# Kernel tuning notes

Measured on AMD Instinct MI355X. Metric: run time of the kernel, lower is better.

## Reference

```python
import jax, jax.numpy as jnp
import numpy as np

N, T, NC, D = 256, 20, 1, 32
NF, Q, VSTEPS, HDYN = 16, 32, 10, 256
HDIM = NF * 64           # n_filt * 4**3
DT = 0.1
BETA = 1.0
LOG2PI = float(np.log(2.0 * np.pi))


def conv2d(x, w, b):
    # k=4, s=2, p=1 : halves spatial dims. x: [B,Cin,H,W], w: [Cout,Cin,4,4]
    y = jax.lax.conv_general_dilated(x, w, (2, 2), [(1, 1), (1, 1)],
                                     dimension_numbers=('NCHW', 'OIHW', 'NCHW'))
    return y + b[None, :, None, None]


def deconv2d(x, w, b):
    # stride-2 transposed conv, doubles spatial dims. w: [Cout,Cin,4,4]
    y = jax.lax.conv_transpose(x, w, (2, 2), 'SAME',
                               dimension_numbers=('NCHW', 'OIHW', 'NCHW'))
    return y + b[None, :, None, None]


def encode(x, C1, c1, C2, c2, C3, c3, Wm, bm, Wl, bl):
    h = jax.nn.relu(conv2d(x, C1, c1))
    h = jax.nn.relu(conv2d(h, C2, c2))
    h = jax.nn.relu(conv2d(h, C3, c3))   # [B, 4*NF, 4, 4]
    h = h.reshape(h.shape[0], -1)        # [B, HDIM]
    return h @ Wm + bm, h @ Wl + bl


def setup_inputs() -> dict:
    key = jax.random.key(0)
    ks = jax.random.split(key, 40)
    r = lambda i, shape, s=0.05: s * jax.random.normal(ks[i], shape, jnp.float32)
    inp = {
        'X': jax.random.uniform(ks[0], (N, T, NC, D, D), jnp.float32),
        'eps_s0': jax.random.normal(ks[1], (N, Q), jnp.float32),
        'eps_v0': jax.random.normal(ks[2], (N, Q), jnp.float32),
        # enc_s (input = 1 frame)
        'Cs1': r(3, (NF, NC, 4, 4)), 'cs1': jnp.zeros((NF,)),
        'Cs2': r(4, (2 * NF, NF, 4, 4)), 'cs2': jnp.zeros((2 * NF,)),
        'Cs3': r(5, (4 * NF, 2 * NF, 4, 4)), 'cs3': jnp.zeros((4 * NF,)),
        'Wsm': r(6, (HDIM, Q)), 'bsm': jnp.zeros((Q,)),
        'Wsl': r(7, (HDIM, Q), 0.01), 'bsl': -1.0 * jnp.ones((Q,)),
        # enc_v (input = v_steps frames stacked as channels)
        'Cv1': r(8, (NF, VSTEPS * NC, 4, 4)), 'cv1': jnp.zeros((NF,)),
        'Cv2': r(9, (2 * NF, NF, 4, 4)), 'cv2': jnp.zeros((2 * NF,)),
        'Cv3': r(10, (4 * NF, 2 * NF, 4, 4)), 'cv3': jnp.zeros((4 * NF,)),
        'Wvm': r(11, (HDIM, Q)), 'bvm': jnp.zeros((Q,)),
        'Wvl': r(12, (HDIM, Q), 0.01), 'bvl': -1.0 * jnp.ones((Q,)),
        # dynamics f : R^{2q} -> R^q (tanh MLP)
        'W1': r(13, (2 * Q, HDYN), 0.1), 'b1': jnp.zeros((HDYN,)),
        'W2': r(14, (HDYN, Q), 0.1), 'b2': jnp.zeros((Q,)),
        # fc3 + decoder
        'Wf': r(15, (Q, HDIM)), 'bf': jnp.zeros((HDIM,)),
        'D1': r(16, (2 * NF, 4 * NF, 4, 4)), 'd1': jnp.zeros((2 * NF,)),
        'D2': r(17, (NF, 2 * NF, 4, 4)), 'd2': jnp.zeros((NF,)),
        'D3': r(18, (NC, NF, 4, 4)), 'd3': jnp.zeros((NC,)),
        'Ndata': 10000,
    }
    return inp


def reference(X, eps_s0, eps_v0,
              Cs1, cs1, Cs2, cs2, Cs3, cs3, Wsm, bsm, Wsl, bsl,
              Cv1, cv1, Cv2, cv2, Cv3, cv3, Wvm, bvm, Wvl, bvl,
              W1, b1, W2, b2, Wf, bf, D1, d1, D2, d2, D3, d3, Ndata):
    Nb, Tt = X.shape[0], X.shape[1]
    # ---- encode z0 = [v0, s0]
    s0_mu, s0_lv = encode(X[:, 0], Cs1, cs1, Cs2, cs2, Cs3, cs3, Wsm, bsm, Wsl, bsl)
    xv = X[:, :VSTEPS].reshape(Nb, VSTEPS * NC, D, D)
    v0_mu, v0_lv = encode(xv, Cv1, cv1, Cv2, cv2, Cv3, cv3, Wvm, bvm, Wvl, bvl)
    s0 = s0_mu + eps_s0 * jnp.exp(s0_lv)
    v0 = v0_mu + eps_v0 * jnp.exp(v0_lv)
    # standard-normal density of the base noise (q dims each)
    logp0 = (-0.5 * jnp.sum(eps_s0 ** 2, -1) - 0.5 * Q * LOG2PI) + \
            (-0.5 * jnp.sum(eps_v0 ** 2, -1) - 0.5 * Q * LOG2PI)
    z0 = jnp.concatenate([v0, s0], axis=1)               # [N,2q]
    qz0_m = jnp.concatenate([v0_mu, s0_mu], axis=1)
    qz0_logv = jnp.concatenate([v0_lv, s0_lv], axis=1)

    # ---- augmented ODE rhs: dz = [f(z), v], dlogp = -tr(df/dv)
    # exact trace for the tanh MLP: J = W2^T diag(1-h^2) W1^T, so
    # tr_{i<q} J = (1-h^2) @ c with c_k = sum_{i<q} W1[i,k] * W2[k,i]
    c = jnp.sum(W1[:Q] * W2.T, axis=0)                   # [HDYN]

    def rhs(vs):
        h = jnp.tanh(vs @ W1 + b1)                       # [N,HDYN]
        dv = h @ W2 + b2                                 # [N,q]
        dvs = jnp.concatenate([dv, vs[:, :Q]], axis=1)   # [N,2q]
        tr = (1.0 - h * h) @ c                           # [N]
        return dvs, -tr

    def rk4_step(carry, _):
        z, lp = carry
        k1z, k1l = rhs(z)
        k2z, k2l = rhs(z + 0.5 * DT * k1z)
        k3z, k3l = rhs(z + 0.5 * DT * k2z)
        k4z, k4l = rhs(z + DT * k3z)
        z2 = z + (DT / 6.0) * (k1z + 2 * k2z + 2 * k3z + k4z)
        lp2 = lp + (DT / 6.0) * (k1l + 2 * k2l + 2 * k3l + k4l)
        return (z2, lp2), (z2, lp2)

    (_, _), (zs, lps) = jax.lax.scan(rk4_step, (z0, logp0), None, length=Tt - 1)
    zt = jnp.concatenate([z0[None], zs], axis=0)         # [T,N,2q]
    logp = jnp.concatenate([logp0[None], lps], axis=0)   # [T,N]
    ztL = jnp.transpose(zt, (1, 0, 2))[None]             # [1,N,T,2q] (L=1)
    logpL = logp.T[None]                                 # [1,N,T]

    # ---- decode positions s_t
    s = ztL[..., Q:].reshape(-1, Q) @ Wf + bf            # [N*T, HDIM]
    h = s.reshape(-1, 4 * NF, 4, 4)
    h = jax.nn.relu(deconv2d(h, D1, d1))                 # [N*T,2NF,8,8]
    h = jax.nn.relu(deconv2d(h, D2, d2))                 # [N*T,NF,16,16]
    Xrec = jax.nn.sigmoid(deconv2d(h, D3, d3))           # [N*T,NC,32,32]
    Xrec = Xrec.reshape(1, Nb, Tt, NC, D, D)

    # ---- ELBO
    log_pzt = -0.5 * jnp.sum(ztL ** 2, -1) - Q * LOG2PI  # N(0,I) over 2q dims
    kl_z = (logpL - log_pzt).sum(2).mean(0)              # [N]
    lhood_L = jnp.log(0.001 + Xrec) * X[None] + jnp.log(1.001 - Xrec) * (1.0 - X[None])
    lhood = lhood_L.sum((2, 3, 4, 5)).mean(0)            # [N]
    kl_w = 0.5 * (jnp.sum(W1 ** 2) + jnp.sum(W2 ** 2))
    Nd = jnp.float32(Ndata)
    lh = Nd * lhood.mean()
    klz = Nd * kl_z.mean()
    elbo = lh - klz - BETA * kl_w
    return Xrec, qz0_m, qz0_logv, ztL, elbo, lh, klz, BETA * kl_w


if __name__ == '__main__':
    outs = reference(**setup_inputs())
    print(outs[0].shape, float(outs[4]))
```

## Files before the change

### kernel.cpp

```cpp
#include <hip/hip_runtime.h>
#include <math.h>

#define N_S 256
#define T_S 20
#define D_S 32
#define NF_S 16
#define Q_S 32
#define HDYN_S 256
#define HDIM_S 1024
#define VSTEPS_S 10
#define DT_S 0.1f
#define LOG2PI_F 1.8378770664093453f

#define OUT_XREC 0
#define OUT_QM   5242880
#define OUT_QLV  5259264
#define OUT_ZT   5275648
#define OUT_SCAL 5603328

#define WS_A1    0
#define WS_A3    0
#define WS_WT1   0
#define WS_WT2   32768
#define WS_WT3   40960
#define WS_A2    1048576
#define WS_S0MU  1572864
#define WS_S0LV  1581056
#define WS_V0MU  1589248
#define WS_V0LV  1597440
#define WS_LOGP  1605632
#define WS_LHOOD 1610752
#define WS_KLZ   1611008
#define WS_KLW   1611264
#define WS_TC    1611520
#define TC_S1 (WS_TC + 0)
#define TC_V1 (WS_TC + 256)
#define TC_S2 (WS_TC + 2816)
#define TC_V2 (WS_TC + 11008)
#define TC_S3 (WS_TC + 19200)
#define TC_V3 (WS_TC + 51968)

__device__ inline void enc_tr(const float* __restrict__ src, float* __restrict__ dst,
                              int e, int CI, int CO) {
    int co = e % CO; int r = e / CO; int tap = r & 15; int ci = r >> 4;
    dst[e] = src[(co * CI + ci) * 16 + tap];
}
__device__ inline void dec_tr(const float* __restrict__ src, float* __restrict__ dst,
                              int e, int CI, int CO) {
    int co = e % CO; int r = e / CO; int ci = r % CI; int tap = r / CI;
    dst[e] = src[(co * CI + ci) * 16 + tap];
}

__global__ __launch_bounds__(256) void prep_enc(
    const float* __restrict__ Cs1, const float* __restrict__ Cv1,
    const float* __restrict__ Cs2, const float* __restrict__ Cv2,
    const float* __restrict__ Cs3, const float* __restrict__ Cv3,
    float* __restrict__ ws)
{
    int idx = blockIdx.x * 256 + threadIdx.x;
    if (blockIdx.x == 0) ws[WS_LHOOD + threadIdx.x] = 0.f;
    if (idx < 256)        enc_tr(Cs1, ws + TC_S1, idx,          1, 16);
    else if (idx < 2816)  enc_tr(Cv1, ws + TC_V1, idx - 256,   10, 16);
    else if (idx < 11008) enc_tr(Cs2, ws + TC_S2, idx - 2816,  16, 32);
    else if (idx < 19200) enc_tr(Cv2, ws + TC_V2, idx - 11008, 16, 32);
    else if (idx < 51968) enc_tr(Cs3, ws + TC_S3, idx - 19200, 32, 64);
    else if (idx < 84736) enc_tr(Cv3, ws + TC_V3, idx - 51968, 32, 64);
}

template<int CIN>
__global__ __launch_bounds__(256) void conv1_lds(
    const float* __restrict__ x, const float* __restrict__ wt,
    const float* __restrict__ bias, float* __restrict__ out)
{
    __shared__ float xin[CIN * 630];
    __shared__ float wl[CIN * 256];
    __shared__ float bl[16];
    int b = blockIdx.x, yh = blockIdx.y, t = threadIdx.x;
    for (int e = t; e < CIN * 576; e += 256) {
        int ci = e / 576;
        int r = (e >> 5) - ci * 18;
        int cx = e & 31;
        int gy = yh * 16 - 1 + r;
        float v = (gy >= 0 && gy < 32) ? x[(size_t)b * 20480 + ci * 1024 + gy * 32 + cx] : 0.f;
        xin[ci * 630 + r * 35 + cx + 1] = v;
    }
    for (int e = t; e < CIN * 18; e += 256) {
        int ci = e / 18, r = e - ci * 18;
        xin[ci * 630 + r * 35 + 0] = 0.f;
        xin[ci * 630 + r * 35 + 33] = 0.f;
    }
    for (int e = t; e < CIN * 256; e += 256) wl[e] = wt[e];
    if (t < 16) bl[t] = bias[t];
    __syncthreads();

    int ocq = t >> 7, p = t & 127;
    int oyl = p >> 4, ox = p & 15;
    float acc[8];
    #pragma unroll
    for (int j = 0; j < 8; j++) acc[j] = bl[ocq * 8 + j];
    for (int ci = 0; ci < CIN; ci++) {
        const float* xc = xin + ci * 630;
        const float* wc = wl + ci * 256 + ocq * 8;
        #pragma unroll
        for (int ky = 0; ky < 4; ky++) {
            const float* xr = xc + (2 * oyl + ky) * 35;
            #pragma unroll
            for (int kx = 0; kx < 4; kx++) {
                float v = xr[2 * ox + kx];
                const float4* w4 = (const float4*)(wc + (ky * 4 + kx) * 16);
                float4 wa = w4[0], wb = w4[1];
                acc[0] = fmaf(v, wa.x, acc[0]);
                acc[1] = fmaf(v, wa.y, acc[1]);
                acc[2] = fmaf(v, wa.z, acc[2]);
                acc[3] = fmaf(v, wa.w, acc[3]);
                acc[4] = fmaf(v, wb.x, acc[4]);
                acc[5] = fmaf(v, wb.y, acc[5]);
                acc[6] = fmaf(v, wb.z, acc[6]);
                acc[7] = fmaf(v, wb.w, acc[7]);
            }
        }
    }
    int oy = yh * 8 + oyl;
    size_t ob = (size_t)b * 4096 + (size_t)(ocq * 8) * 256 + oy * 16 + ox;
    #pragma unroll
    for (int j = 0; j < 8; j++) out[ob + (size_t)j * 256] = fmaxf(acc[j], 0.f);
}

__global__ __launch_bounds__(256) void conv2_lds(
    const float* __restrict__ a1, const float* __restrict__ wt,
    const float* __restrict__ bias, float* __restrict__ out)
{
    __shared__ float xin[16 * 272];
    __shared__ float wl[4096];
    __shared__ float bl[16];
    int b = blockIdx.x, h = blockIdx.y, t = threadIdx.x;
    for (int e = t; e < 4096; e += 256) {
        int ci = e >> 8, r = e & 255, iy = r >> 4, ix = r & 15;
        xin[ci * 272 + iy * 17 + ix] = a1[(size_t)b * 4096 + e];
    }
    for (int e = t; e < 4096; e += 256) {
        int ci = e >> 8, r = e & 255, tap = r >> 4, oc = r & 15;
        wl[e] = wt[ci * 512 + tap * 32 + h * 16 + oc];
    }
    if (t < 16) bl[t] = bias[h * 16 + t];
    __syncthreads();

    int ocq = t >> 6, p = t & 63;
    int pa = p >> 3, pb = p & 7;
    float acc[4];
    #pragma unroll
    for (int j = 0; j < 4; j++) acc[j] = bl[ocq * 4 + j];
    for (int ci = 0; ci < 16; ci++) {
        const float* xc = xin + ci * 272;
        const float* wc = wl + ci * 256 + ocq * 4;
        #pragma unroll
        for (int ky = 0; ky < 4; ky++) {
            int iy = 2 * pa - 1 + ky;
            if ((unsigned)iy >= 16u) continue;
            const float* xr = xc + iy * 17;
            #pragma unroll
            for (int kx = 0; kx < 4; kx++) {
                int ix = 2 * pb - 1 + kx;
                if ((unsigned)ix >= 16u) continue;
                float v = xr[ix];
                float4 wv = *(const float4*)(wc + (ky * 4 + kx) * 16);
                acc[0] = fmaf(v, wv.x, acc[0]);
                acc[1] = fmaf(v, wv.y, acc[1]);
                acc[2] = fmaf(v, wv.z, acc[2]);
                acc[3] = fmaf(v, wv.w, acc[3]);
            }
        }
    }
    size_t ob = (size_t)b * 2048 + (size_t)(h * 16 + ocq * 4) * 64 + pa * 8 + pb;
    #pragma unroll
    for (int j = 0; j < 4; j++) out[ob + (size_t)j * 64] = fmaxf(acc[j], 0.f);
}

__global__ __launch_bounds__(256) void conv3_lds(
    const float* __restrict__ a2, const float* __restrict__ wt,
    const float* __restrict__ bias, float* __restrict__ out)
{
    __shared__ float xin[32 * 72];
    __shared__ float wl[16384];
    __shared__ float bl[32];
    int b = blockIdx.x, h = blockIdx.y, t = threadIdx.x;
    for (int e = t; e < 2048; e += 256) {
        int ci = e >> 6, r = e & 63, iy = r >> 3, ix = r & 7;
        xin[ci * 72 + iy * 9 + ix] = a2[(size_t)b * 2048 + e];
    }
    for (int e4 = t; e4 < 4096; e4 += 256) {
        int grp = e4 >> 3, c4 = e4 & 7;
        ((float4*)wl)[e4] = ((const float4*)(wt + grp * 64 + h * 32))[c4];
    }
    if (t < 32) bl[t] = bias[h * 32 + t];
    __syncthreads();

    int ocq = t >> 4, p = t & 15;
    int pa = p >> 2, pb = p & 3;
    float a0 = bl[ocq * 2], a1 = bl[ocq * 2 + 1];
    for (int ci = 0; ci < 32; ci++) {
        const float* xc = xin + ci * 72;
        const float* wc = wl + ci * 512 + ocq * 2;
        #pragma unroll
        for (int ky = 0; ky < 4; ky++) {
            int iy = 2 * pa - 1 + ky;
            if ((unsigned)iy >= 8u) continue;
            const float* xr = xc + iy * 9;
            #pragma unroll
            for (int kx = 0; kx < 4; kx++) {
                int ix = 2 * pb - 1 + kx;
                if ((unsigned)ix >= 8u) continue;
                float v = xr[ix];
                float2 wv = *(const float2*)(wc + (ky * 4 + kx) * 32);
                a0 = fmaf(v, wv.x, a0);
                a1 = fmaf(v, wv.y, a1);
            }
        }
    }
    size_t ob = (size_t)b * 1024 + (size_t)(h * 32 + ocq * 2) * 16 + pa * 4 + pb;
    out[ob] = fmaxf(a0, 0.f);
    out[ob + 16] = fmaxf(a1, 0.f);
}

__global__ __launch_bounds__(256) void fc_enc2(
    const float* __restrict__ h,
    const float* __restrict__ Wm, const float* __restrict__ bm,
    const float* __restrict__ Wl, const float* __restrict__ bl,
    float* __restrict__ mu, float* __restrict__ lv)
{
    __shared__ float pm[8][32], pl[8][32];
    int b = blockIdx.x, t = threadIdx.x;
    int q = t & 31, c = t >> 5;
    const float* hb = h + (size_t)b * HDIM_S + c * 128;
    const float* wmp = Wm + (c * 128) * Q_S + q;
    const float* wlp = Wl + (c * 128) * Q_S + q;
    float am = 0.f, al = 0.f;
    #pragma unroll 4
    for (int k = 0; k < 128; k++) {
        float hv = hb[k];
        am = fmaf(hv, wmp[k * Q_S], am);
        al = fmaf(hv, wlp[k * Q_S], al);
    }
    pm[c][q] = am; pl[c][q] = al;
    __syncthreads();
    if (t < 32) {
        float s = bm[t];
        #pragma unroll
        for (int c2 = 0; c2 < 8; c2++) s += pm[c2][t];
        mu[b * Q_S + t] = s;
    } else if (t < 64) {
        int qq = t - 32;
        float s = bl[qq];
        #pragma unroll
        for (int c2 = 0; c2 < 8; c2++) s += pl[c2][qq];
        lv[b * Q_S + qq] = s;
    }
}

__global__ __launch_bounds__(256) void reparam_prep(
    const float* __restrict__ s0mu, const float* __restrict__ s0lv,
    const float* __restrict__ v0mu, const float* __restrict__ v0lv,
    const float* __restrict__ eps_s, const float* __restrict__ eps_v,
    const float* __restrict__ D1, const float* __restrict__ D2,
    const float* __restrict__ D3,
    float* __restrict__ ws,
    float* __restrict__ qm, float* __restrict__ qlv,
    float* __restrict__ ztL, float* __restrict__ logp)
{
    int n = blockIdx.x, t = threadIdx.x;
    int idx = n * 256 + t;
    if (idx < 32768)      dec_tr(D1, ws + WS_WT1, idx,         64, 32);
    else if (idx < 40960) dec_tr(D2, ws + WS_WT2, idx - 32768, 32, 16);
    else if (idx < 41216) dec_tr(D3, ws + WS_WT3, idx - 40960, 16, 1);
    if (t < 64) {
        int q = t & 31;
        float mu, lvv, ep;
        if (t < 32) { mu = v0mu[n*32+q]; lvv = v0lv[n*32+q]; ep = eps_v[n*32+q]; }
        else        { mu = s0mu[n*32+q]; lvv = s0lv[n*32+q]; ep = eps_s[n*32+q]; }
        float zv = fmaf(ep, expf(lvv), mu);
        qm[n*64 + t]  = mu;
        qlv[n*64 + t] = lvv;
        ztL[(size_t)n * T_S * 64 + t] = zv;
        float e2 = ep * ep;
        #pragma unroll
        for (int off = 32; off; off >>= 1) e2 += __shfl_down(e2, off, 64);
        if (t == 0) logp[n * T_S] = -0.5f * e2 - Q_S * LOG2PI_F;
    }
}

__global__ __launch_bounds__(256) void ode_kernel(
    const float* __restrict__ W1, const float* __restrict__ b1,
    const float* __restrict__ W2, const float* __restrict__ b2,
    float* __restrict__ ztL, float* __restrict__ logp)
{
    __shared__ float W2s[HDYN_S * Q_S];
    __shared__ float zeval[64];
    __shared__ float hsh[HDYN_S];
    __shared__ float dvred[HDYN_S];
    __shared__ float red4[4];
    int n = blockIdx.x;
    int t = threadIdx.x;

    for (int i = t; i < HDYN_S * Q_S; i += 256) W2s[i] = W2[i];
    float w1r[64];
    #pragma unroll
    for (int j = 0; j < 64; j++) w1r[j] = W1[j * HDYN_S + t];
    float b1r = b1[t];
    __syncthreads();
    float ck = 0.f;
    #pragma unroll
    for (int i = 0; i < Q_S; i++) ck = fmaf(w1r[i], W2s[t * Q_S + i], ck);

    size_t zoff = (size_t)n * T_S * 64;
    float zj = 0.f, ksumj = 0.f, zevalj = 0.f, lp = 0.f, lsum = 0.f;
    if (t < 64) { zj = ztL[zoff + t]; zevalj = zj; zeval[t] = zj; }
    if (t == 0) lp = logp[n * T_S];

    const float wc[4] = {1.f, 2.f, 2.f, 1.f};
    const float ac[3] = {0.5f * DT_S, 0.5f * DT_S, DT_S};

    for (int step = 1; step < T_S; step++) {
        for (int e = 0; e < 4; e++) {
            __syncthreads();
            float p0 = 0.f, p1 = 0.f, p2 = 0.f, p3 = 0.f;
            #pragma unroll
            for (int j = 0; j < 16; j++) {
                p0 = fmaf(zeval[j],      w1r[j],      p0);
                p1 = fmaf(zeval[j + 16], w1r[j + 16], p1);
                p2 = fmaf(zeval[j + 32], w1r[j + 32], p2);
                p3 = fmaf(zeval[j + 48], w1r[j + 48], p3);
            }
            float pre = b1r + ((p0 + p1) + (p2 + p3));
            float hk = tanhf(pre);
            hsh[t] = hk;
            float gk = (1.f - hk * hk) * ck;
            #pragma unroll
            for (int off = 32; off; off >>= 1) gk += __shfl_down(gk, off, 64);
            if ((t & 63) == 0) red4[t >> 6] = gk;
            __syncthreads();
            {
                int i = t & 31, p = t >> 5;
                float a0 = 0.f, a1 = 0.f;
                #pragma unroll
                for (int kk = 0; kk < 16; kk++) {
                    a0 = fmaf(hsh[p * 32 + kk],      W2s[(p * 32 + kk) * Q_S + i],      a0);
                    a1 = fmaf(hsh[p * 32 + 16 + kk], W2s[(p * 32 + 16 + kk) * Q_S + i], a1);
                }
                dvred[t] = a0 + a1;
            }
            __syncthreads();
            if (t < 64) {
                float tr = red4[0] + red4[1] + red4[2] + red4[3];
                float zv_shfl = __shfl(zevalj, (t >= 32) ? (t - 32) : t, 64);
                float kzv;
                if (t < 32) {
                    float dvi = b2[t];
                    #pragma unroll
                    for (int p = 0; p < 8; p++) dvi += dvred[p * 32 + t];
                    kzv = dvi;
                } else kzv = zv_shfl;
                if (e == 0) ksumj = kzv; else ksumj = fmaf(wc[e], kzv, ksumj);
                if (t == 0) { float kl = -tr; lsum = (e == 0) ? kl : fmaf(wc[e], kl, lsum); }
                if (e < 3) {
                    zevalj = fmaf(ac[e], kzv, zj);
                    zeval[t] = zevalj;
                } else {
                    zj = fmaf(DT_S / 6.f, ksumj, zj);
                    zevalj = zj; zeval[t] = zj;
                    ztL[zoff + step * 64 + t] = zj;
                    if (t == 0) { lp = fmaf(DT_S / 6.f, lsum, lp); logp[n * T_S + step] = lp; }
                }
            }
        }
    }
}

__global__ __launch_bounds__(256) void decoder5(
    const float* __restrict__ ztL, const float* __restrict__ Wf, const float* __restrict__ bf,
    const float* __restrict__ wt1, const float* __restrict__ d1,
    const float* __restrict__ wt2, const float* __restrict__ d2,
    const float* __restrict__ wt3, const float* __restrict__ d3,
    const float* __restrict__ X, float* __restrict__ Xrec, float* __restrict__ lhood)
{
    __shared__ float zs[32];
    __shared__ float h1p[5200];
    __shared__ float u2[5264];
    __shared__ float sh4[4];
    float* slp = u2;
    float* h2p = u2;
    float* xst = h1p;
    const int bidx = blockIdx.x;
    const int t = threadIdx.x;
    const int wu = __builtin_amdgcn_readfirstlane(t >> 6);
    const int l = t & 63;
    const int py = wu >> 1, px = wu & 1;

    if (t < 32) zs[t] = ztL[(size_t)bidx * 64 + 32 + t];
    {
        float4 z4 = make_float4(0.f, 0.f, 0.f, 0.f);
        for (int e = t; e < 1316; e += 256) ((float4*)u2)[e] = z4;
        for (int e = t; e < 1300; e += 256) ((float4*)h1p)[e] = z4;
    }
    __syncthreads();

    {
        float4 acc = ((const float4*)bf)[t];
        const float4* Wf4 = (const float4*)Wf;
        #pragma unroll 4
        for (int q = 0; q < 32; q++) {
            float zq = zs[q];
            float4 wv = Wf4[q * 256 + t];
            acc.x = fmaf(zq, wv.x, acc.x);
            acc.y = fmaf(zq, wv.y, acc.y);
            acc.z = fmaf(zq, wv.z, acc.z);
            acc.w = fmaf(zq, wv.w, acc.w);
        }
        int k0 = t * 4;
        int ci = k0 >> 4, p0 = k0 & 15;
        int iy = p0 >> 2;
        float vv[4] = {acc.x, acc.y, acc.z, acc.w};
        #pragma unroll
        for (int j = 0; j < 4; j++)
            slp[(iy + 1) * 412 + (j + 1) * 68 + ci] = vv[j];
    }
    __syncthreads();

    {
        int ocq = l >> 3;
        int pp = l & 7;
        int a_ = pp >> 1, b2 = pp & 1;
        float acc0[4], acc1[4];
        #pragma unroll
        for (int j = 0; j < 4; j++) { acc0[j] = d1[ocq * 4 + j]; acc1[j] = acc0[j]; }
        #pragma unroll
        for (int sy = 0; sy < 2; sy++) {
            int ky = py + 2 * sy;
            int iy = a_ + py + sy - 1;
            #pragma unroll
            for (int sx = 0; sx < 2; sx++) {
                int kx = px + 2 * sx;
                int ix0 = 2 * b2 + px + sx - 1;
                const float4* ip0 = (const float4*)(slp + (iy + 1) * 412 + (ix0 + 1) * 68);
                const float4* ip1 = (const float4*)((const float*)ip0 + 68);
                const float* wb = wt1 + (ky * 4 + kx) * 2048 + ocq * 4;
                #pragma unroll 4
                for (int cc = 0; cc < 16; cc++) {
                    float4 va = ip0[cc];
                    float4 vb = ip1[cc];
                    float av[4] = {va.x, va.y, va.z, va.w};
                    float bv[4] = {vb.x, vb.y, vb.z, vb.w};
                    #pragma unroll
                    for (int r = 0; r < 4; r++) {
                        float4 wv = *(const float4*)(wb + (cc * 4 + r) * 32);
                        acc0[0] = fmaf(av[r], wv.x, acc0[0]); acc1[0] = fmaf(bv[r], wv.x, acc1[0]);
                        acc0[1] = fmaf(av[r], wv.y, acc0[1]); acc1[1] = fmaf(bv[r], wv.y, acc1[1]);
                        acc0[2] = fmaf(av[r], wv.z, acc0[2]); acc1[2] = fmaf(bv[r], wv.z, acc1[2]);
                        acc0[3] = fmaf(av[r], wv.w, acc0[3]); acc1[3] = fmaf(bv[r], wv.w, acc1[3]);
                    }
                }
            }
        }
        float* hp = h1p + (py * 2 + px) * 1300;
        int ox0 = 2 * b2, ox1 = ox0 + 1;
        float4 r0, r1;
        r0.x = fmaxf(acc0[0],0.f); r0.y = fmaxf(acc0[1],0.f); r0.z = fmaxf(acc0[2],0.f); r0.w = fmaxf(acc0[3],0.f);
        r1.x = fmaxf(acc1[0],0.f); r1.y = fmaxf(acc1[1],0.f); r1.z = fmaxf(acc1[2],0.f); r1.w = fmaxf(acc1[3],0.f);
        *(float4*)(hp + (a_ + 1) * 216 + (ox0 + 1) * 36 + ocq * 4) = r0;
        *(float4*)(hp + (a_ + 1) * 216 + (ox1 + 1) * 36 + ocq * 4) = r1;
    }
    __syncthreads();

    {
        int a = l >> 3, b = l & 7;
        float acc[16];
        #pragma unroll
        for (int j = 0; j < 16; j++) acc[j] = d2[j];
        #pragma unroll
        for (int sy = 0; sy < 2; sy++) {
            int ky = py + 2 * sy;
            int iyf = a + py + sy - 1;
            int pyi = iyf & 1, ly = iyf >> 1;
            #pragma unroll
            for (int sx = 0; sx < 2; sx++) {
                int kx = px + 2 * sx;
                int ixf = b + px + sx - 1;
                int pxi = ixf & 1, lx = ixf >> 1;
                const float4* ip4 = (const float4*)(h1p + (pyi * 2 + pxi) * 1300
                                                    + (ly + 1) * 216 + (lx + 1) * 36);
                const float* wb = wt2 + (ky * 4 + kx) * 512;
                #pragma unroll 2
                for (int cc = 0; cc < 8; cc++) {
                    float4 v = ip4[cc];
                    float vv[4] = {v.x, v.y, v.z, v.w};
                    #pragma unroll
                    for (int r = 0; r < 4; r++) {
                        const float4* wq = (const float4*)(wb + (cc * 4 + r) * 16);
                        float4 w0 = wq[0], w1 = wq[1], w2 = wq[2], w3 = wq[3];
                        float vr = vv[r];
                        acc[0]  = fmaf(vr, w0.x, acc[0]);
                        acc[1]  = fmaf(vr, w0.y, acc[1]);
                        acc[2]  = fmaf(vr, w0.z, acc[2]);
                        acc[3]  = fmaf(vr, w0.w, acc[3]);
                        acc[4]  = fmaf(vr, w1.x, acc[4]);
                        acc[5]  = fmaf(vr, w1.y, acc[5]);
                        acc[6]  = fmaf(vr, w1.z, acc[6]);
                        acc[7]  = fmaf(vr, w1.w, acc[7]);
                        acc[8]  = fmaf(vr, w2.x, acc[8]);
                        acc[9]  = fmaf(vr, w2.y, acc[9]);
                        acc[10] = fmaf(vr, w2.z, acc[10]);
                        acc[11] = fmaf(vr, w2.w, acc[11]);
                        acc[12] = fmaf(vr, w3.x, acc[12]);
                        acc[13] = fmaf(vr, w3.y, acc[13]);
                        acc[14] = fmaf(vr, w3.z, acc[14]);
                        acc[15] = fmaf(vr, w3.w, acc[15]);
                    }
                }
            }
        }
        __syncthreads();
        float* hq = h2p + (py * 2 + px) * 1316 + a * 164 + b * 20;
        #pragma unroll
        for (int j = 0; j < 4; j++) {
            float4 r;
            r.x = fmaxf(acc[j*4+0], 0.f);
            r.y = fmaxf(acc[j*4+1], 0.f);
            r.z = fmaxf(acc[j*4+2], 0.f);
            r.w = fmaxf(acc[j*4+3], 0.f);
            *(float4*)(hq + j * 4) = r;
        }
    }
    __syncthreads();

    {
        int oy2 = l >> 2, b3 = l & 3;
        float acc[4];
        float d30 = d3[0];
        #pragma unroll
        for (int k = 0; k < 4; k++) acc[k] = d30;
        #pragma unroll
        for (int sy = 0; sy < 2; sy++) {
            int ky = py + 2 * sy;
            int iy = oy2 + py + sy - 1;
            if ((unsigned)iy >= 16u) continue;
            int pyi = iy & 1, ly = iy >> 1;
            #pragma unroll
            for (int sx = 0; sx < 2; sx++) {
                int kx = px + 2 * sx;
                int cx = px + sx - 1;
                const float* wvp = wt3 + (ky * 4 + kx) * 16;
                #pragma unroll
                for (int k = 0; k < 4; k++) {
                    int ix = b3 + 4 * k + cx;
                    if ((unsigned)ix >= 16u) continue;
                    int pxi = ix & 1, lx = ix >> 1;
                    const float4* in4 = (const float4*)(h2p + (pyi*2+pxi)*1316 + ly*164 + lx*20);
                    #pragma unroll
                    for (int cc = 0; cc < 4; cc++) {
                        float4 v = in4[cc];
                        float4 wq = ((const float4*)wvp)[cc];
                        acc[k] = fmaf(v.x, wq.x, acc[k]);
                        acc[k] = fmaf(v.y, wq.y, acc[k]);
                        acc[k] = fmaf(v.z, wq.z, acc[k]);
                        acc[k] = fmaf(v.w, wq.w, acc[k]);
                    }
                }
            }
        }
        int oy = 2 * oy2 + py;
        #pragma unroll
        for (int k = 0; k < 4; k++) {
            int ox = 2 * (b3 + 4 * k) + px;
            xst[oy * 36 + ox] = 1.f / (1.f + expf(-acc[k]));
        }
    }
    __syncthreads();

    {
        int row = t >> 3, col = (t & 7) * 4;
        float4 xr4 = *(const float4*)(xst + row * 36 + col);
        *(float4*)(Xrec + (size_t)bidx * 1024 + t * 4) = xr4;
        float4 xi4 = *(const float4*)(X + (size_t)bidx * 1024 + t * 4);
        float ll = 0.f;
        ll += logf(0.001f + xr4.x) * xi4.x + logf(1.001f - xr4.x) * (1.f - xi4.x);
        ll += logf(0.001f + xr4.y) * xi4.y + logf(1.001f - xr4.y) * (1.f - xi4.y);
        ll += logf(0.001f + xr4.z) * xi4.z + logf(1.001f - xr4.z) * (1.f - xi4.z);
        ll += logf(0.001f + xr4.w) * xi4.w + logf(1.001f - xr4.w) * (1.f - xi4.w);
        #pragma unroll
        for (int off = 32; off; off >>= 1) ll += __shfl_down(ll, off, 64);
        if ((t & 63) == 0) sh4[t >> 6] = ll;
    }
    __syncthreads();
    if (t == 0) atomicAdd(&lhood[bidx / T_S], sh4[0] + sh4[1] + sh4[2] + sh4[3]);
}

__global__ __launch_bounds__(64) void klz_kernel(
    const float* __restrict__ ztL, const float* __restrict__ logp, float* __restrict__ klz)
{
    int n = blockIdx.x, t = threadIdx.x;
    float v = 0.f;
    if (t < T_S) {
        const float* z = ztL + ((size_t)n * T_S + t) * 64;
        float s2 = 0.f;
        #pragma unroll
        for (int j = 0; j < 64; j++) s2 = fmaf(z[j], z[j], s2);
        v = logp[n * T_S + t] - (-0.5f * s2 - Q_S * LOG2PI_F);
    }
    #pragma unroll
    for (int off = 32; off; off >>= 1) v += __shfl_down(v, off, 64);
    if (t == 0) klz[n] = v;
}

__global__ __launch_bounds__(256) void final2(
    const float* __restrict__ lhood, const float* __restrict__ klz,
    const float* __restrict__ W1, const float* __restrict__ W2,
    const int* __restrict__ Ndata, float* __restrict__ outs)
{
    __shared__ float shA[4], shB[4], shC[4];
    int t = threadIdx.x;
    float a = lhood[t];
    float b = klz[t];
    float c = 0.f;
    for (int i = t; i < 64 * HDYN_S; i += 256) c = fmaf(W1[i], W1[i], c);
    for (int i = t; i < HDYN_S * Q_S; i += 256) c = fmaf(W2[i], W2[i], c);
    #pragma unroll
    for (int off = 32; off; off >>= 1) {
        a += __shfl_down(a, off, 64);
        b += __shfl_down(b, off, 64);
        c += __shfl_down(c, off, 64);
    }
    if ((t & 63) == 0) { shA[t >> 6] = a; shB[t >> 6] = b; shC[t >> 6] = c; }
    __syncthreads();
    if (t == 0) {
        float Nd = (float)Ndata[0];
        float lh = Nd * ((shA[0] + shA[1] + shA[2] + shA[3]) / 256.f);
        float kz = Nd * ((shB[0] + shB[1] + shB[2] + shB[3]) / 256.f);
        float bkw = 0.5f * (shC[0] + shC[1] + shC[2] + shC[3]);
        outs[0] = lh - kz - bkw;
        outs[1] = lh;
        outs[2] = kz;
        outs[3] = bkw;
    }
}

extern "C" void kernel_launch(void* const* d_in, const int* in_sizes, int n_in,
                              void* d_out, int out_size, void* d_ws, size_t ws_size,
                              hipStream_t stream) {
    const float* X      = (const float*)d_in[0];
    const float* eps_s0 = (const float*)d_in[1];
    const float* eps_v0 = (const float*)d_in[2];
    const float* Cs1 = (const float*)d_in[3],  *cs1 = (const float*)d_in[4];
    const float* Cs2 = (const float*)d_in[5],  *cs2 = (const float*)d_in[6];
    const float* Cs3 = (const float*)d_in[7],  *cs3 = (const float*)d_in[8];
    const float* Wsm = (const float*)d_in[9],  *bsm = (const float*)d_in[10];
    const float* Wsl = (const float*)d_in[11], *bsl = (const float*)d_in[12];
    const float* Cv1 = (const float*)d_in[13], *cv1 = (const float*)d_in[14];
    const float* Cv2 = (const float*)d_in[15], *cv2 = (const float*)d_in[16];
    const float* Cv3 = (const float*)d_in[17], *cv3 = (const float*)d_in[18];
    const float* Wvm = (const float*)d_in[19], *bvm = (const float*)d_in[20];
    const float* Wvl = (const float*)d_in[21], *bvl = (const float*)d_in[22];
    const float* W1  = (const float*)d_in[23], *b1  = (const float*)d_in[24];
    const float* W2  = (const float*)d_in[25], *b2  = (const float*)d_in[26];
    const float* Wf  = (const float*)d_in[27], *bf  = (const float*)d_in[28];
    const float* D1  = (const float*)d_in[29], *d1  = (const float*)d_in[30];
    const float* D2  = (const float*)d_in[31], *d2  = (const float*)d_in[32];
    const float* D3  = (const float*)d_in[33], *d3  = (const float*)d_in[34];
    const int*   Ndata = (const int*)d_in[35];

    float* out = (float*)d_out;
    float* ws  = (float*)d_ws;

    prep_enc<<<331, 256, 0, stream>>>(Cs1, Cv1, Cs2, Cv2, Cs3, Cv3, ws);

    conv1_lds<1><<<dim3(256, 2), 256, 0, stream>>>(X, ws + TC_S1, cs1, ws + WS_A1);
    conv2_lds<<<dim3(256, 2), 256, 0, stream>>>(ws + WS_A1, ws + TC_S2, cs2, ws + WS_A2);
    conv3_lds<<<dim3(256, 2), 256, 0, stream>>>(ws + WS_A2, ws + TC_S3, cs3, ws + WS_A3);
    fc_enc2<<<256, 256, 0, stream>>>(ws + WS_A3, Wsm, bsm, Wsl, bsl, ws + WS_S0MU, ws + WS_S0LV);

    conv1_lds<10><<<dim3(256, 2), 256, 0, stream>>>(X, ws + TC_V1, cv1, ws + WS_A1);
    conv2_lds<<<dim3(256, 2), 256, 0, stream>>>(ws + WS_A1, ws + TC_V2, cv2, ws + WS_A2);
    conv3_lds<<<dim3(256, 2), 256, 0, stream>>>(ws + WS_A2, ws + TC_V3, cv3, ws + WS_A3);
    fc_enc2<<<256, 256, 0, stream>>>(ws + WS_A3, Wvm, bvm, Wvl, bvl, ws + WS_V0MU, ws + WS_V0LV);

    reparam_prep<<<256, 256, 0, stream>>>(ws + WS_S0MU, ws + WS_S0LV, ws + WS_V0MU, ws + WS_V0LV,
                                          eps_s0, eps_v0, D1, D2, D3, ws,
                                          out + OUT_QM, out + OUT_QLV,
                                          out + OUT_ZT, ws + WS_LOGP);

    ode_kernel<<<256, 256, 0, stream>>>(W1, b1, W2, b2, out + OUT_ZT, ws + WS_LOGP);

    decoder5<<<5120, 256, 0, stream>>>(out + OUT_ZT, Wf, bf,
                                       ws + WS_WT1, d1, ws + WS_WT2, d2, ws + WS_WT3, d3,
                                       X, out + OUT_XREC, ws + WS_LHOOD);

    klz_kernel<<<256, 64, 0, stream>>>(out + OUT_ZT, ws + WS_LOGP, ws + WS_KLZ);
    final2<<<1, 256, 0, stream>>>(ws + WS_LHOOD, ws + WS_KLZ, W1, W2, Ndata,
                                  out + OUT_SCAL);
}
```

Baseline: 583.3 us.

## Fuse KL-z reduction into ODE kernel, compact decoder LDS, regrid conv3

Three changes land together. The separate klz_kernel launch goes away, and the per-step KL term is now accumulated inside the ODE integration loop. The decoder stores intermediates in LDS without padding halos and sends out-of-bounds reads to a small zeroed pad region, which removes the per-block LDS zero-fill and one barrier. conv3 now launches twice as many blocks, each producing one output channel per thread with two interleaved accumulators, which halves per-block LDS weight staging. Risks are extra shuffles in the ODE's serial loop and possible LDS hazards from removing the decoder barrier.

After: 611.1 us. 4.8% more time.

```diff
diff --git a/kernel.cpp b/kernel.cpp
--- a/kernel.cpp
+++ b/kernel.cpp
@@ -31,7 +31,6 @@
 #define WS_LOGP  1605632
 #define WS_LHOOD 1610752
 #define WS_KLZ   1611008
-#define WS_KLW   1611264
 #define WS_TC    1611520
 #define TC_S1 (WS_TC + 0)
 #define TC_V1 (WS_TC + 256)
@@ -176,50 +175,47 @@
     for (int j = 0; j < 4; j++) out[ob + (size_t)j * 64] = fmaxf(acc[j], 0.f);
 }
 
-__global__ __launch_bounds__(256) void conv3_lds(
+__global__ __launch_bounds__(256) void conv3b(
     const float* __restrict__ a2, const float* __restrict__ wt,
     const float* __restrict__ bias, float* __restrict__ out)
 {
     __shared__ float xin[32 * 72];
-    __shared__ float wl[16384];
-    __shared__ float bl[32];
+    __shared__ float wl[8192];
+    __shared__ float bl[16];
     int b = blockIdx.x, h = blockIdx.y, t = threadIdx.x;
     for (int e = t; e < 2048; e += 256) {
         int ci = e >> 6, r = e & 63, iy = r >> 3, ix = r & 7;
         xin[ci * 72 + iy * 9 + ix] = a2[(size_t)b * 2048 + e];
     }
-    for (int e4 = t; e4 < 4096; e4 += 256) {
-        int grp = e4 >> 3, c4 = e4 & 7;
-        ((float4*)wl)[e4] = ((const float4*)(wt + grp * 64 + h * 32))[c4];
-    }
-    if (t < 32) bl[t] = bias[h * 32 + t];
-    __syncthreads();
-
-    int ocq = t >> 4, p = t & 15;
+    for (int e = t; e < 8192; e += 256) {
+        int ci = e >> 8, r = e & 255, tap = r >> 4, oc = r & 15;
+        wl[e] = wt[ci * 1024 + tap * 64 + h * 16 + oc];
+    }
+    if (t < 16) bl[t] = bias[h * 16 + t];
+    __syncthreads();
+
+    int oc = t >> 4, p = t & 15;
     int pa = p >> 2, pb = p & 3;
-    float a0 = bl[ocq * 2], a1 = bl[ocq * 2 + 1];
-    for (int ci = 0; ci < 32; ci++) {
-        const float* xc = xin + ci * 72;
-        const float* wc = wl + ci * 512 + ocq * 2;
+    float s0 = bl[oc], s1 = 0.f;
+    for (int ci = 0; ci < 32; ci += 2) {
+        const float* xc0 = xin + ci * 72;
+        const float* wc0 = wl + ci * 256 + oc;
         #pragma unroll
         for (int ky = 0; ky < 4; ky++) {
             int iy = 2 * pa - 1 + ky;
             if ((unsigned)iy >= 8u) continue;
-            const float* xr = xc + iy * 9;
+            const float* xr0 = xc0 + iy * 9;
             #pragma unroll
             for (int kx = 0; kx < 4; kx++) {
                 int ix = 2 * pb - 1 + kx;
                 if ((unsigned)ix >= 8u) continue;
-                float v = xr[ix];
-                float2 wv = *(const float2*)(wc + (ky * 4 + kx) * 32);
-                a0 = fmaf(v, wv.x, a0);
-                a1 = fmaf(v, wv.y, a1);
-            }
-        }
-    }
-    size_t ob = (size_t)b * 1024 + (size_t)(h * 32 + ocq * 2) * 16 + pa * 4 + pb;
-    out[ob] = fmaxf(a0, 0.f);
-    out[ob + 16] = fmaxf(a1, 0.f);
+                int wi = (ky * 4 + kx) * 16;
+                s0 = fmaf(xr0[ix],      wc0[wi],       s0);
+                s1 = fmaf(xr0[72 + ix], wc0[256 + wi], s1);
+            }
+        }
+    }
+    out[(size_t)b * 1024 + h * 256 + t] = fmaxf(s0 + s1, 0.f);
 }
 
 __global__ __launch_bounds__(256) void fc_enc2(
@@ -291,7 +287,7 @@
 __global__ __launch_bounds__(256) void ode_kernel(
     const float* __restrict__ W1, const float* __restrict__ b1,
     const float* __restrict__ W2, const float* __restrict__ b2,
-    float* __restrict__ ztL, float* __restrict__ logp)
+    float* __restrict__ ztL, float* __restrict__ logp, float* __restrict__ klz)
 {
     __shared__ float W2s[HDYN_S * Q_S];
     __shared__ float zeval[64];
@@ -312,9 +308,15 @@
     for (int i = 0; i < Q_S; i++) ck = fmaf(w1r[i], W2s[t * Q_S + i], ck);
 
     size_t zoff = (size_t)n * T_S * 64;
-    float zj = 0.f, ksumj = 0.f, zevalj = 0.f, lp = 0.f, lsum = 0.f;
+    float zj = 0.f, ksumj = 0.f, zevalj = 0.f, lp = 0.f, lsum = 0.f, klzacc = 0.f;
     if (t < 64) { zj = ztL[zoff + t]; zevalj = zj; zeval[t] = zj; }
     if (t == 0) lp = logp[n * T_S];
+    {
+        float e2z = zj * zj;
+        #pragma unroll
+        for (int off = 32; off; off >>= 1) e2z += __shfl_down(e2z, off, 64);
+        if (t == 0) klzacc = lp + 0.5f * e2z + Q_S * LOG2PI_F;
+    }
 
     const float wc[4] = {1.f, 2.f, 2.f, 1.f};
     const float ac[3] = {0.5f * DT_S, 0.5f * DT_S, DT_S};
@@ -368,14 +370,22 @@
                     zj = fmaf(DT_S / 6.f, ksumj, zj);
                     zevalj = zj; zeval[t] = zj;
                     ztL[zoff + step * 64 + t] = zj;
-                    if (t == 0) { lp = fmaf(DT_S / 6.f, lsum, lp); logp[n * T_S + step] = lp; }
+                    float e2z = zj * zj;
+                    #pragma unroll
+                    for (int off = 32; off; off >>= 1) e2z += __shfl_down(e2z, off, 64);
+                    if (t == 0) {
+                        lp = fmaf(DT_S / 6.f, lsum, lp);
+                        logp[n * T_S + step] = lp;
+                        klzacc += lp + 0.5f * e2z + Q_S * LOG2PI_F;
+                    }
                 }
             }
         }
     }
-}
-
-__global__ __launch_bounds__(256) void decoder5(
+    if (t == 0) klz[n] = klzacc;
+}
+
+__global__ __launch_bounds__(256) void decoder6(
     const float* __restrict__ ztL, const float* __restrict__ Wf, const float* __restrict__ bf,
     const float* __restrict__ wt1, const float* __restrict__ d1,
     const float* __restrict__ wt2, const float* __restrict__ d2,
@@ -383,12 +393,12 @@
     const float* __restrict__ X, float* __restrict__ Xrec, float* __restrict__ lhood)
 {
     __shared__ float zs[32];
-    __shared__ float h1p[5200];
-    __shared__ float u2[5264];
+    __shared__ float h1s[2360];
+    __shared__ float u2[5340];
     __shared__ float sh4[4];
     float* slp = u2;
     float* h2p = u2;
-    float* xst = h1p;
+    float* xst = h1s;
     const int bidx = blockIdx.x;
     const int t = threadIdx.x;
     const int wu = __builtin_amdgcn_readfirstlane(t >> 6);
@@ -396,11 +406,8 @@
     const int py = wu >> 1, px = wu & 1;
 
     if (t < 32) zs[t] = ztL[(size_t)bidx * 64 + 32 + t];
-    {
-        float4 z4 = make_float4(0.f, 0.f, 0.f, 0.f);
-        for (int e = t; e < 1316; e += 256) ((float4*)u2)[e] = z4;
-        for (int e = t; e < 1300; e += 256) ((float4*)h1p)[e] = z4;
-    }
+    if (t < 68) u2[5264 + t] = 0.f;
+    if (t < 36) h1s[2320 + t] = 0.f;
     __syncthreads();
 
     {
@@ -421,7 +428,7 @@
         float vv[4] = {acc.x, acc.y, acc.z, acc.w};
         #pragma unroll
         for (int j = 0; j < 4; j++)
-            slp[(iy + 1) * 412 + (j + 1) * 68 + ci] = vv[j];
+            slp[(iy * 4 + j) * 68 + ci] = vv[j];
     }
     __syncthreads();
 
@@ -436,12 +443,16 @@
         for (int sy = 0; sy < 2; sy++) {
             int ky = py + 2 * sy;
             int iy = a_ + py + sy - 1;
+            bool rowok = (unsigned)iy < 4u;
             #pragma unroll
             for (int sx = 0; sx < 2; sx++) {
                 int kx = px + 2 * sx;
                 int ix0 = 2 * b2 + px + sx - 1;
-                const float4* ip0 = (const float4*)(slp + (iy + 1) * 412 + (ix0 + 1) * 68);
-                const float4* ip1 = (const float4*)((const float*)ip0 + 68);
+                int ix1 = ix0 + 1;
+                int off0 = (rowok && (unsigned)ix0 < 4u) ? (iy * 4 + ix0) * 68 : 5264;
+                int off1 = (rowok && (unsigned)ix1 < 4u) ? (iy * 4 + ix1) * 68 : 5264;
+                const float4* ip0 = (const float4*)(u2 + off0);
+                const float4* ip1 = (const float4*)(u2 + off1);
                 const float* wb = wt1 + (ky * 4 + kx) * 2048 + ocq * 4;
                 #pragma unroll 4
                 for (int cc = 0; cc < 16; cc++) {
@@ -460,13 +471,13 @@
                 }
             }
         }
-        float* hp = h1p + (py * 2 + px) * 1300;
+        float* hp = h1s + (py * 2 + px) * 580;
         int ox0 = 2 * b2, ox1 = ox0 + 1;
         float4 r0, r1;
         r0.x = fmaxf(acc0[0],0.f); r0.y = fmaxf(acc0[1],0.f); r0.z = fmaxf(acc0[2],0.f); r0.w = fmaxf(acc0[3],0.f);
         r1.x = fmaxf(acc1[0],0.f); r1.y = fmaxf(acc1[1],0.f); r1.z = fmaxf(acc1[2],0.f); r1.w = fmaxf(acc1[3],0.f);
-        *(float4*)(hp + (a_ + 1) * 216 + (ox0 + 1) * 36 + ocq * 4) = r0;
-        *(float4*)(hp + (a_ + 1) * 216 + (ox1 + 1) * 36 + ocq * 4) = r1;
+        *(float4*)(hp + (a_ * 4 + ox0) * 36 + ocq * 4) = r0;
+        *(float4*)(hp + (a_ * 4 + ox1) * 36 + ocq * 4) = r1;
     }
     __syncthreads();
 
@@ -480,13 +491,15 @@
             int ky = py + 2 * sy;
             int iyf = a + py + sy - 1;
             int pyi = iyf & 1, ly = iyf >> 1;
+            bool yok = (unsigned)iyf < 8u;
             #pragma unroll
             for (int sx = 0; sx < 2; sx++) {
                 int kx = px + 2 * sx;
                 int ixf = b + px + sx - 1;
                 int pxi = ixf & 1, lx = ixf >> 1;
-                const float4* ip4 = (const float4*)(h1p + (pyi * 2 + pxi) * 1300
-                                                    + (ly + 1) * 216 + (lx + 1) * 36);
+                int off = (yok && (unsigned)ixf < 8u)
+                          ? ((pyi * 2 + pxi) * 580 + (ly * 4 + lx) * 36) : 2320;
+                const float4* ip4 = (const float4*)(h1s + off);
                 const float* wb = wt2 + (ky * 4 + kx) * 512;
                 #pragma unroll 2
                 for (int cc = 0; cc < 8; cc++) {
@@ -517,7 +530,6 @@
                 }
             }
         }
-        __syncthreads();
         float* hq = h2p + (py * 2 + px) * 1316 + a * 164 + b * 20;
         #pragma unroll
         for (int j = 0; j < 4; j++) {
@@ -591,23 +603,6 @@
     }
     __syncthreads();
     if (t == 0) atomicAdd(&lhood[bidx / T_S], sh4[0] + sh4[1] + sh4[2] + sh4[3]);
-}
-
-__global__ __launch_bounds__(64) void klz_kernel(
-    const float* __restrict__ ztL, const float* __restrict__ logp, float* __restrict__ klz)
-{
-    int n = blockIdx.x, t = threadIdx.x;
-    float v = 0.f;
-    if (t < T_S) {
-        const float* z = ztL + ((size_t)n * T_S + t) * 64;
-        float s2 = 0.f;
-        #pragma unroll
-        for (int j = 0; j < 64; j++) s2 = fmaf(z[j], z[j], s2);
-        v = logp[n * T_S + t] - (-0.5f * s2 - Q_S * LOG2PI_F);
-    }
-    #pragma unroll
-    for (int off = 32; off; off >>= 1) v += __shfl_down(v, off, 64);
-    if (t == 0) klz[n] = v;
 }
 
 __global__ __launch_bounds__(256) void final2(
@@ -673,12 +668,12 @@
 
     conv1_lds<1><<<dim3(256, 2), 256, 0, stream>>>(X, ws + TC_S1, cs1, ws + WS_A1);
     conv2_lds<<<dim3(256, 2), 256, 0, stream>>>(ws + WS_A1, ws + TC_S2, cs2, ws + WS_A2);
-    conv3_lds<<<dim3(256, 2), 256, 0, stream>>>(ws + WS_A2, ws + TC_S3, cs3, ws + WS_A3);
+    conv3b<<<dim3(256, 4), 256, 0, stream>>>(ws + WS_A2, ws + TC_S3, cs3, ws + WS_A3);
     fc_enc2<<<256, 256, 0, stream>>>(ws + WS_A3, Wsm, bsm, Wsl, bsl, ws + WS_S0MU, ws + WS_S0LV);
 
     conv1_lds<10><<<dim3(256, 2), 256, 0, stream>>>(X, ws + TC_V1, cv1, ws + WS_A1);
     conv2_lds<<<dim3(256, 2), 256, 0, stream>>>(ws + WS_A1, ws + TC_V2, cv2, ws + WS_A2);
-    conv3_lds<<<dim3(256, 2), 256, 0, stream>>>(ws + WS_A2, ws + TC_V3, cv3, ws + WS_A3);
+    conv3b<<<dim3(256, 4), 256, 0, stream>>>(ws + WS_A2, ws + TC_V3, cv3, ws + WS_A3);
     fc_enc2<<<256, 256, 0, stream>>>(ws + WS_A3, Wvm, bvm, Wvl, bvl, ws + WS_V0MU, ws + WS_V0LV);
 
     reparam_prep<<<256, 256, 0, stream>>>(ws + WS_S0MU, ws + WS_S0LV, ws + WS_V0MU, ws + WS_V0LV,
@@ -686,13 +681,13 @@
                                           out + OUT_QM, out + OUT_QLV,
                                           out + OUT_ZT, ws + WS_LOGP);
 
-    ode_kernel<<<256, 256, 0, stream>>>(W1, b1, W2, b2, out + OUT_ZT, ws + WS_LOGP);
-
-    decoder5<<<5120, 256, 0, stream>>>(out + OUT_ZT, Wf, bf,
+    ode_kernel<<<256, 256, 0, stream>>>(W1, b1, W2, b2, out + OUT_ZT, ws + WS_LOGP,
+                                        ws + WS_KLZ);
+
+    decoder6<<<5120, 256, 0, stream>>>(out + OUT_ZT, Wf, bf,
                                        ws + WS_WT1, d1, ws + WS_WT2, d2, ws + WS_WT3, d3,
                                        X, out + OUT_XREC, ws + WS_LHOOD);
 
-    klz_kernel<<<256, 64, 0, stream>>>(out + OUT_ZT, ws + WS_LOGP, ws + WS_KLZ);
     final2<<<1, 256, 0, stream>>>(ws + WS_LHOOD, ws + WS_KLZ, W1, W2, Ndata,
                                   out + OUT_SCAL);
 }
```
